# Performance work log

Hardware: AMD Instinct MI355X
Metric: run time of the kernel (lower is better)

The kernel has to match this reference:

```python
import jax, jax.numpy as jnp
import numpy as np

N_EMBD = 1024
N_HEAD = 16


def setup_inputs() -> dict:
    key = jax.random.key(0)
    ks = jax.random.split(key, 9)
    s = 1.0 / np.sqrt(N_EMBD)
    d = {
        "x": jax.random.normal(ks[0], (4, 2048, N_EMBD), dtype=jnp.float32),
        "Wq": jax.random.normal(ks[1], (N_EMBD, N_EMBD), dtype=jnp.float32) * s,
        "bq": jnp.zeros((N_EMBD,), dtype=jnp.float32),
        "Wk": jax.random.normal(ks[2], (N_EMBD, N_EMBD), dtype=jnp.float32) * s,
        "bk": jnp.zeros((N_EMBD,), dtype=jnp.float32),
        "Wv": jax.random.normal(ks[3], (N_EMBD, N_EMBD), dtype=jnp.float32) * s,
        "bv": jnp.zeros((N_EMBD,), dtype=jnp.float32),
        "Wp": jax.random.normal(ks[4], (N_EMBD, N_EMBD), dtype=jnp.float32) * s,
        "bp": jnp.zeros((N_EMBD,), dtype=jnp.float32),
    }
    return d


def reference(x, Wq, bq, Wk, bk, Wv, bv, Wp, bp):
    B, T, C = x.shape
    H = N_HEAD
    D = C // H  # head dim
    # QKV projections -> [B, H, T, D]
    def split_heads(y):
        return y.reshape(B, T, H, D).transpose(0, 2, 1, 3)
    q = split_heads(x @ Wq + bq)
    k = split_heads(x @ Wk + bk)
    v = split_heads(x @ Wv + bv)
    # full (non-causal) attention, scaled by 1/sqrt(D)
    att = jnp.einsum("bhtd,bhsd->bhts", q, k) * (1.0 / np.sqrt(D))
    att = jax.nn.softmax(att, axis=-1)  # dropout is identity (p=0 / eval)
    out = jnp.einsum("bhts,bhsd->bhtd", att, v)
    out = out.transpose(0, 2, 1, 3).reshape(B, T, C)
    return out @ Wp + bp
```

## Files before the change

kernel.cpp:

```cpp
#include <hip/hip_runtime.h>
#include <math.h>

#define B_ 4
#define T_ 2048
#define C_ 1024
#define H_ 16
#define D_ 64
#define M_ (B_ * T_)

#define QSCALE 0.18033688011112042f

using bf16x8 = __attribute__((ext_vector_type(8))) short;
using f32x4  = __attribute__((ext_vector_type(4))) float;

__device__ __forceinline__ unsigned short f2bf(float f) {
  unsigned u = __float_as_uint(f);
  unsigned r = u + 0x7FFFu + ((u >> 16) & 1u);
  return (unsigned short)(r >> 16);
}
__device__ __forceinline__ float bf2f(unsigned short h) {
  return __uint_as_float(((unsigned)h) << 16);
}
__device__ __forceinline__ unsigned cvtpk_bf16(float lo, float hi) {
  unsigned r;
  asm volatile("v_cvt_pk_bf16_f32 %0, %1, %2" : "=v"(r) : "v"(lo), "v"(hi));
  return r;
}

__global__ __launch_bounds__(256) void conv_x(const float* __restrict__ x,
                                              unsigned short* __restrict__ hi,
                                              unsigned short* __restrict__ lo) {
  const size_t i = ((size_t)blockIdx.x * 256 + threadIdx.x) * 4;
  const float4 v = *(const float4*)&x[i];
  ushort4 h, l;
  h.x = f2bf(v.x); l.x = f2bf(v.x - bf2f(h.x));
  h.y = f2bf(v.y); l.y = f2bf(v.y - bf2f(h.y));
  h.z = f2bf(v.z); l.z = f2bf(v.z - bf2f(h.z));
  h.w = f2bf(v.w); l.w = f2bf(v.w - bf2f(h.w));
  *(ushort4*)&hi[i] = h;
  *(ushort4*)&lo[i] = l;
}

__global__ __launch_bounds__(256) void conv_wT(const float* __restrict__ W,
                                               unsigned short* __restrict__ hi,
                                               unsigned short* __restrict__ lo,
                                               int n_off) {
  __shared__ float t[64][65];
  const int k0 = blockIdx.y * 64, n0 = blockIdx.x * 64;
  const int lr = threadIdx.x >> 4;
  const int lc4 = (threadIdx.x & 15) * 4;
#pragma unroll
  for (int i = 0; i < 4; ++i) {
    const int r = lr + 16 * i;
    const float4 v = *(const float4*)&W[(size_t)(k0 + r) * 1024 + n0 + lc4];
    t[r][lc4 + 0] = v.x; t[r][lc4 + 1] = v.y;
    t[r][lc4 + 2] = v.z; t[r][lc4 + 3] = v.w;
  }
  __syncthreads();
#pragma unroll
  for (int i = 0; i < 4; ++i) {
    const int nr = lr + 16 * i;
    ushort4 h, l;
    float a0 = t[lc4 + 0][nr], a1 = t[lc4 + 1][nr];
    float a2 = t[lc4 + 2][nr], a3 = t[lc4 + 3][nr];
    h.x = f2bf(a0); l.x = f2bf(a0 - bf2f(h.x));
    h.y = f2bf(a1); l.y = f2bf(a1 - bf2f(h.y));
    h.z = f2bf(a2); l.z = f2bf(a2 - bf2f(h.z));
    h.w = f2bf(a3); l.w = f2bf(a3 - bf2f(h.w));
    const size_t o = (size_t)(n_off + n0 + nr) * 1024 + k0 + lc4;
    *(ushort4*)&hi[o] = h;
    *(ushort4*)&lo[o] = l;
  }
}

template <int MODE>
__global__ __launch_bounds__(256) void gemm_mfma(
    const unsigned short* __restrict__ Ahi, const unsigned short* __restrict__ Alo,
    const unsigned short* __restrict__ Bhi, const unsigned short* __restrict__ Blo,
    const float* __restrict__ bias0, const float* __restrict__ bias1,
    const float* __restrict__ bias2,
    void* P0, void* P1, void* P2, void* P3, void* P4, void* P5) {
  __shared__ __align__(16) unsigned short AhS[128 * 32];
  __shared__ __align__(16) unsigned short AlS[128 * 32];
  __shared__ __align__(16) unsigned short BhS[128 * 32];
  __shared__ __align__(16) unsigned short BlS[128 * 32];

  const int tid = threadIdx.x;
  const int lane = tid & 63;
  const int wid = tid >> 6;

  const int GX = (MODE == 1) ? 24 : 8;
  const int nwg = GX * 64;
  int lin = blockIdx.x + blockIdx.y * GX;
  lin = (lin & 7) * (nwg >> 3) + (lin >> 3);
  const int m0 = (lin / GX) * 128, n0 = (lin % GX) * 128;

  const int wm = (wid >> 1) * 64, wn = (wid & 1) * 64;

  f32x4 acc[4][4] = {};

  const int srow = lane >> 2;
  const int sc = lane & 3;
  const int fr = lane & 15;
  const int q = lane >> 4;

  for (int k0 = 0; k0 < 1024; k0 += 32) {
    __syncthreads();
#pragma unroll
    for (int c = 0; c < 2; ++c) {
      const int chunk = wid * 2 + c;
      const int row = chunk * 16 + srow;
      const int kch = sc ^ ((row >> 1) & 3);
      const size_t ao = (size_t)(m0 + row) * 1024 + k0 + kch * 8;
      const size_t bo = (size_t)(n0 + row) * 1024 + k0 + kch * 8;
      __builtin_amdgcn_global_load_lds(
          (const __attribute__((address_space(1))) void*)(Ahi + ao),
          (__attribute__((address_space(3))) void*)(AhS + chunk * 512), 16, 0, 0);
      __builtin_amdgcn_global_load_lds(
          (const __attribute__((address_space(1))) void*)(Alo + ao),
          (__attribute__((address_space(3))) void*)(AlS + chunk * 512), 16, 0, 0);
      __builtin_amdgcn_global_load_lds(
          (const __attribute__((address_space(1))) void*)(Bhi + bo),
          (__attribute__((address_space(3))) void*)(BhS + chunk * 512), 16, 0, 0);
      __builtin_amdgcn_global_load_lds(
          (const __attribute__((address_space(1))) void*)(Blo + bo),
          (__attribute__((address_space(3))) void*)(BlS + chunk * 512), 16, 0, 0);
    }
    __syncthreads();

    bf16x8 afh[4], bfh[4], afl[4], bfl[4];
#pragma unroll
    for (int i = 0; i < 4; ++i) {
      const int arow = wm + i * 16 + fr;
      const int aoff = arow * 32 + (q ^ ((arow >> 1) & 3)) * 8;
      afh[i] = *(const bf16x8*)(AhS + aoff);
      const int brow = wn + i * 16 + fr;
      const int boff = brow * 32 + (q ^ ((brow >> 1) & 3)) * 8;
      bfh[i] = *(const bf16x8*)(BhS + boff);
    }
#pragma unroll
    for (int i = 0; i < 4; ++i)
#pragma unroll
      for (int j = 0; j < 4; ++j)
        acc[i][j] = __builtin_amdgcn_mfma_f32_16x16x32_bf16(afh[i], bfh[j], acc[i][j], 0, 0, 0);
#pragma unroll
    for (int i = 0; i < 4; ++i) {
      const int brow = wn + i * 16 + fr;
      bfl[i] = *(const bf16x8*)(BlS + brow * 32 + (q ^ ((brow >> 1) & 3)) * 8);
    }
#pragma unroll
    for (int i = 0; i < 4; ++i)
#pragma unroll
      for (int j = 0; j < 4; ++j)
        acc[i][j] = __builtin_amdgcn_mfma_f32_16x16x32_bf16(afh[i], bfl[j], acc[i][j], 0, 0, 0);
#pragma unroll
    for (int i = 0; i < 4; ++i) {
      const int arow = wm + i * 16 + fr;
      afl[i] = *(const bf16x8*)(AlS + arow * 32 + (q ^ ((arow >> 1) & 3)) * 8);
    }
#pragma unroll
    for (int i = 0; i < 4; ++i)
#pragma unroll
      for (int j = 0; j < 4; ++j)
        acc[i][j] = __builtin_amdgcn_mfma_f32_16x16x32_bf16(afl[i], bfh[j], acc[i][j], 0, 0, 0);
  }

  if (MODE == 0) {
    float* out = (float*)P0;
#pragma unroll
    for (int i = 0; i < 4; ++i)
#pragma unroll
      for (int j = 0; j < 4; ++j)
#pragma unroll
        for (int r = 0; r < 4; ++r) {
          const int m = m0 + wm + i * 16 + q * 4 + r;
          const int n = n0 + wn + j * 16 + fr;
          out[(size_t)m * 1024 + n] = acc[i][j][r] + bias0[n];
        }
  } else {
#pragma unroll
    for (int i = 0; i < 4; ++i) {
#pragma unroll
      for (int j = 0; j < 4; ++j) {
        const int n = n0 + wn + j * 16 + fr;
        const int seg = n >> 10, ww = n & 1023, h = ww >> 6, d = ww & 63;
        const float bv = ((seg == 0) ? bias0 : (seg == 1) ? bias1 : bias2)[ww];
        const int mb = m0 + wm + i * 16 + q * 4;
        const int b = mb >> 11, t0 = mb & 2047;
        unsigned short hv[4], lv[4];
#pragma unroll
        for (int r = 0; r < 4; ++r) {
          float v = acc[i][j][r] + bv;
          if (seg == 0) v *= QSCALE;
          hv[r] = f2bf(v);
          lv[r] = f2bf(v - bf2f(hv[r]));
        }
        if (seg == 2) {
          const size_t o = (((size_t)b * H_ + h) * D_ + d) * T_ + t0;
          ushort4 h4, l4;
          h4.x = hv[0]; h4.y = hv[1]; h4.z = hv[2]; h4.w = hv[3];
          l4.x = lv[0]; l4.y = lv[1]; l4.z = lv[2]; l4.w = lv[3];
          *(ushort4*)&((unsigned short*)P4)[o] = h4;
          *(ushort4*)&((unsigned short*)P5)[o] = l4;
        } else {
          unsigned short* Hq = (unsigned short*)((seg == 0) ? P0 : P2);
          unsigned short* Lq = (unsigned short*)((seg == 0) ? P1 : P3);
          const size_t ob = ((size_t)b * H_ + h) * T_;
#pragma unroll
          for (int r = 0; r < 4; ++r) {
            const size_t o = (ob + t0 + r) * D_ + d;
            Hq[o] = hv[r];
            Lq[o] = lv[r];
          }
        }
      }
    }
  }
}

__global__ __launch_bounds__(256) void flash_mfma(
    const unsigned short* __restrict__ Qhi, const unsigned short* __restrict__ Qlo,
    const unsigned short* __restrict__ Khi, const unsigned short* __restrict__ Klo,
    const unsigned short* __restrict__ Vthi, const unsigned short* __restrict__ Vtlo,
    unsigned short* __restrict__ chi, unsigned short* __restrict__ clo) {
  __shared__ __align__(16) unsigned short KhiS[64 * 64];
  __shared__ __align__(16) unsigned short KloS[64 * 64];
  __shared__ __align__(16) unsigned short VhiS[64 * 64];
  __shared__ __align__(16) unsigned short VloS[64 * 64];
  __shared__ __align__(16) unsigned short PsT[4][32 * 64];

  const int tid = threadIdx.x;
  const int lane = tid & 63;
  const int w = tid >> 6;

  int lin = blockIdx.x + blockIdx.y * 16;
  lin = (lin & 7) * 128 + (lin >> 3);
  const int bh = lin >> 4;
  const int q0 = (lin & 15) * 128;

  const int b = bh >> 4, h = bh & 15;
  const int fr = lane & 15, q = lane >> 4;

  const size_t kbase = (size_t)bh * T_ * D_;
  const size_t vbase = (size_t)bh * D_ * T_;

  bf16x8 qhi[2][2], qlo[2][2];
#pragma unroll
  for (int g = 0; g < 2; ++g)
#pragma unroll
    for (int ks = 0; ks < 2; ++ks) {
      const size_t a = kbase + (size_t)(q0 + w * 32 + g * 16 + fr) * D_ + ks * 32 + q * 8;
      qhi[g][ks] = *(const bf16x8*)(Qhi + a);
      qlo[g][ks] = *(const bf16x8*)(Qlo + a);
    }

  unsigned short* psw = &PsT[w][0];

  f32x4 accO[4][2] = {};
  float lsum[2] = {};

  for (int s0 = 0; s0 < T_; s0 += 64) {
    __syncthreads();
#pragma unroll
    for (int c = 0; c < 2; ++c) {
      const int ci = w * 128 + c * 64 + lane;
      const int row = ci >> 3, slot = ci & 7;
      const int kch = slot ^ (row & 7);
      const int ldsb = (w * 128 + c * 64) * 8;
      const unsigned short* sk = Khi + kbase + (size_t)(s0 + row) * D_ + kch * 8;
      __builtin_amdgcn_global_load_lds(
          (const __attribute__((address_space(1))) void*)sk,
          (__attribute__((address_space(3))) void*)(KhiS + ldsb), 16, 0, 0);
      const unsigned short* sk2 = Klo + kbase + (size_t)(s0 + row) * D_ + kch * 8;
      __builtin_amdgcn_global_load_lds(
          (const __attribute__((address_space(1))) void*)sk2,
          (__attribute__((address_space(3))) void*)(KloS + ldsb), 16, 0, 0);
      const unsigned short* sv = Vthi + vbase + (size_t)row * T_ + s0 + kch * 8;
      __builtin_amdgcn_global_load_lds(
          (const __attribute__((address_space(1))) void*)sv,
          (__attribute__((address_space(3))) void*)(VhiS + ldsb), 16, 0, 0);
      const unsigned short* sv2 = Vtlo + vbase + (size_t)row * T_ + s0 + kch * 8;
      __builtin_amdgcn_global_load_lds(
          (const __attribute__((address_space(1))) void*)sv2,
          (__attribute__((address_space(3))) void*)(VloS + ldsb), 16, 0, 0);
    }
    __syncthreads();

    f32x4 accS[4][2] = {};
#pragma unroll
    for (int sj = 0; sj < 4; ++sj) {
      bf16x8 khf[2], klf[2];
#pragma unroll
      for (int ks = 0; ks < 2; ++ks) {
        const int rs = sj * 16 + fr;
        const int off = rs * 64 + ((ks * 4 + q) ^ (rs & 7)) * 8;
        khf[ks] = *(const bf16x8*)(KhiS + off);
        klf[ks] = *(const bf16x8*)(KloS + off);
      }
#pragma unroll
      for (int g = 0; g < 2; ++g)
#pragma unroll
        for (int ks = 0; ks < 2; ++ks) {
          accS[sj][g] = __builtin_amdgcn_mfma_f32_16x16x32_bf16(khf[ks], qhi[g][ks], accS[sj][g], 0, 0, 0);
          accS[sj][g] = __builtin_amdgcn_mfma_f32_16x16x32_bf16(khf[ks], qlo[g][ks], accS[sj][g], 0, 0, 0);
          accS[sj][g] = __builtin_amdgcn_mfma_f32_16x16x32_bf16(klf[ks], qhi[g][ks], accS[sj][g], 0, 0, 0);
        }
    }

#pragma unroll
    for (int g = 0; g < 2; ++g) {
      const int qc = g * 16 + fr;
#pragma unroll
      for (int sj = 0; sj < 4; ++sj) {
        const float p0 = __builtin_amdgcn_exp2f(accS[sj][g][0]);
        const float p1 = __builtin_amdgcn_exp2f(accS[sj][g][1]);
        const float p2 = __builtin_amdgcn_exp2f(accS[sj][g][2]);
        const float p3 = __builtin_amdgcn_exp2f(accS[sj][g][3]);
        lsum[g] += (p0 + p1) + (p2 + p3);
        uint2 pk;
        pk.x = cvtpk_bf16(p0, p1);
        pk.y = cvtpk_bf16(p2, p3);
        const int off = (qc * 128 + sj * 32 + q * 8) ^ ((fr & 7) << 4);
        *(uint2*)((char*)psw + off) = pk;
      }
    }

    asm volatile("s_waitcnt lgkmcnt(0)" ::: "memory");
    __builtin_amdgcn_sched_barrier(0);

    bf16x8 pb[2][2];
#pragma unroll
    for (int g = 0; g < 2; ++g)
#pragma unroll
      for (int ks = 0; ks < 2; ++ks) {
        const int off = ((g * 16 + fr) * 128 + ks * 64 + q * 16) ^ ((fr & 7) << 4);
        pb[g][ks] = *(const bf16x8*)((char*)psw + off);
      }
#pragma unroll
    for (int j = 0; j < 4; ++j) {
      bf16x8 vh[2], vl[2];
#pragma unroll
      for (int ks = 0; ks < 2; ++ks) {
        const int rd = j * 16 + fr;
        const int off = rd * 64 + ((ks * 4 + q) ^ (rd & 7)) * 8;
        vh[ks] = *(const bf16x8*)(VhiS + off);
        vl[ks] = *(const bf16x8*)(VloS + off);
      }
#pragma unroll
      for (int g = 0; g < 2; ++g)
#pragma unroll
        for (int ks = 0; ks < 2; ++ks) {
          accO[j][g] = __builtin_amdgcn_mfma_f32_16x16x32_bf16(vh[ks], pb[g][ks], accO[j][g], 0, 0, 0);
          accO[j][g] = __builtin_amdgcn_mfma_f32_16x16x32_bf16(vl[ks], pb[g][ks], accO[j][g], 0, 0, 0);
        }
    }
  }

#pragma unroll
  for (int g = 0; g < 2; ++g) {
    float rs = lsum[g];
    rs += __shfl_xor(rs, 16);
    rs += __shfl_xor(rs, 32);
    const float inv = 1.0f / rs;
    const int t = q0 + w * 32 + g * 16 + fr;
    const size_t rowb = ((size_t)b * T_ + t) * C_ + h * D_;
#pragma unroll
    for (int j = 0; j < 4; ++j) {
      ushort4 h4, l4;
      float v0 = accO[j][g][0] * inv, v1 = accO[j][g][1] * inv;
      float v2 = accO[j][g][2] * inv, v3 = accO[j][g][3] * inv;
      h4.x = f2bf(v0); l4.x = f2bf(v0 - bf2f(h4.x));
      h4.y = f2bf(v1); l4.y = f2bf(v1 - bf2f(h4.y));
      h4.z = f2bf(v2); l4.z = f2bf(v2 - bf2f(h4.z));
      h4.w = f2bf(v3); l4.w = f2bf(v3 - bf2f(h4.w));
      const size_t idx = rowb + j * 16 + q * 4;
      *(ushort4*)&chi[idx] = h4;
      *(ushort4*)&clo[idx] = l4;
    }
  }
}

extern "C" void kernel_launch(void* const* d_in, const int* in_sizes, int n_in,
                              void* d_out, int out_size, void* d_ws,
                              size_t ws_size, hipStream_t stream) {
  const float* x = (const float*)d_in[0];
  const float* Wq = (const float*)d_in[1];
  const float* bq = (const float*)d_in[2];
  const float* Wk = (const float*)d_in[3];
  const float* bk = (const float*)d_in[4];
  const float* Wv = (const float*)d_in[5];
  const float* bv = (const float*)d_in[6];
  const float* Wp = (const float*)d_in[7];
  const float* bp = (const float*)d_in[8];
  float* out = (float*)d_out;

  char* w = (char*)d_ws;
  unsigned short* xhi = (unsigned short*)w;     w += (size_t)M_ * C_ * 2;
  unsigned short* xlo = (unsigned short*)w;     w += (size_t)M_ * C_ * 2;
  unsigned short* Wqkv_hi = (unsigned short*)w; w += (size_t)3 * C_ * C_ * 2;
  unsigned short* Wqkv_lo = (unsigned short*)w; w += (size_t)3 * C_ * C_ * 2;
  unsigned short* Wp_hi = (unsigned short*)w;   w += (size_t)C_ * C_ * 2;
  unsigned short* Wp_lo = (unsigned short*)w;   w += (size_t)C_ * C_ * 2;
  unsigned short* Qhi = (unsigned short*)w;     w += (size_t)M_ * C_ * 2;
  unsigned short* Qlo = (unsigned short*)w;     w += (size_t)M_ * C_ * 2;
  unsigned short* Khi = (unsigned short*)w;     w += (size_t)M_ * C_ * 2;
  unsigned short* Klo = (unsigned short*)w;     w += (size_t)M_ * C_ * 2;
  unsigned short* Vthi = (unsigned short*)w;    w += (size_t)M_ * C_ * 2;
  unsigned short* Vtlo = (unsigned short*)w;    w += (size_t)M_ * C_ * 2;
  unsigned short* chi = (unsigned short*)w;     w += (size_t)M_ * C_ * 2;
  unsigned short* clo = (unsigned short*)w;     w += (size_t)M_ * C_ * 2;

  const dim3 blk(256);

  conv_x<<<dim3((M_ * C_) / (4 * 256)), blk, 0, stream>>>(x, xhi, xlo);
  conv_wT<<<dim3(16, 16), blk, 0, stream>>>(Wq, Wqkv_hi, Wqkv_lo, 0);
  conv_wT<<<dim3(16, 16), blk, 0, stream>>>(Wk, Wqkv_hi, Wqkv_lo, 1024);
  conv_wT<<<dim3(16, 16), blk, 0, stream>>>(Wv, Wqkv_hi, Wqkv_lo, 2048);
  conv_wT<<<dim3(16, 16), blk, 0, stream>>>(Wp, Wp_hi, Wp_lo, 0);

  gemm_mfma<1><<<dim3(3072 / 128, M_ / 128), blk, 0, stream>>>(
      xhi, xlo, Wqkv_hi, Wqkv_lo, bq, bk, bv,
      Qhi, Qlo, Khi, Klo, Vthi, Vtlo);

  flash_mfma<<<dim3(T_ / 128, B_ * H_), blk, 0, stream>>>(
      Qhi, Qlo, Khi, Klo, Vthi, Vtlo, chi, clo);

  gemm_mfma<0><<<dim3(1024 / 128, M_ / 128), blk, 0, stream>>>(
      chi, clo, Wp_hi, Wp_lo, bp, bp, bp,
      out, nullptr, nullptr, nullptr, nullptr, nullptr);

  (void)in_sizes; (void)n_in; (void)out_size; (void)ws_size;
}
```

Before: 522.3 us.

## Double-buffer K/V tiles in flash attention with async global-to-LDS prefetch

Doubles the K/V hi/lo LDS buffers and issues the next tile's global_load_lds before computing on the current one. A vmcnt(8) wait plus raw s_barrier replaces the two __syncthreads per iteration, so load latency can overlap the MFMA work. This doubles K/V LDS use (32KB to 64KB plus the P buffers), which may lower occupancy. The manual waitcnt accounting also depends on no other vector-memory ops being in flight.

```diff
diff --git a/kernel.cpp b/kernel.cpp
--- a/kernel.cpp
+++ b/kernel.cpp
@@ -223,10 +223,10 @@
     const unsigned short* __restrict__ Khi, const unsigned short* __restrict__ Klo,
     const unsigned short* __restrict__ Vthi, const unsigned short* __restrict__ Vtlo,
     unsigned short* __restrict__ chi, unsigned short* __restrict__ clo) {
-  __shared__ __align__(16) unsigned short KhiS[64 * 64];
-  __shared__ __align__(16) unsigned short KloS[64 * 64];
-  __shared__ __align__(16) unsigned short VhiS[64 * 64];
-  __shared__ __align__(16) unsigned short VloS[64 * 64];
+  __shared__ __align__(16) unsigned short KhiS[2][64 * 64];
+  __shared__ __align__(16) unsigned short KloS[2][64 * 64];
+  __shared__ __align__(16) unsigned short VhiS[2][64 * 64];
+  __shared__ __align__(16) unsigned short VloS[2][64 * 64];
   __shared__ __align__(16) unsigned short PsT[4][32 * 64];
 
   const int tid = threadIdx.x;
@@ -244,6 +244,51 @@
   const size_t kbase = (size_t)bh * T_ * D_;
   const size_t vbase = (size_t)bh * D_ * T_;
 
+  const int ci0 = w * 128 + lane;
+  const int srow0 = ci0 >> 3, sslot0 = ci0 & 7;
+  const int skch0 = sslot0 ^ (srow0 & 7);
+  const int ci1 = ci0 + 64;
+  const int srow1 = ci1 >> 3, sslot1 = ci1 & 7;
+  const int skch1 = sslot1 ^ (srow1 & 7);
+  const int ldsb0 = (w * 128) * 8;
+  const int ldsb1 = (w * 128 + 64) * 8;
+
+#define STAGE_TILE(buf, s0)                                                      \
+  do {                                                                           \
+    const unsigned short* k0p = Khi + kbase + (size_t)((s0) + srow0) * D_ + skch0 * 8; \
+    const unsigned short* k1p = Klo + kbase + (size_t)((s0) + srow0) * D_ + skch0 * 8; \
+    const unsigned short* v0p = Vthi + vbase + (size_t)srow0 * T_ + (s0) + skch0 * 8;  \
+    const unsigned short* v1p = Vtlo + vbase + (size_t)srow0 * T_ + (s0) + skch0 * 8;  \
+    __builtin_amdgcn_global_load_lds(                                            \
+        (const __attribute__((address_space(1))) void*)k0p,                      \
+        (__attribute__((address_space(3))) void*)(KhiS[buf] + ldsb0), 16, 0, 0); \
+    __builtin_amdgcn_global_load_lds(                                            \
+        (const __attribute__((address_space(1))) void*)k1p,                      \
+        (__attribute__((address_space(3))) void*)(KloS[buf] + ldsb0), 16, 0, 0); \
+    __builtin_amdgcn_global_load_lds(                                            \
+        (const __attribute__((address_space(1))) void*)v0p,                      \
+        (__attribute__((address_space(3))) void*)(VhiS[buf] + ldsb0), 16, 0, 0); \
+    __builtin_amdgcn_global_load_lds(                                            \
+        (const __attribute__((address_space(1))) void*)v1p,                      \
+        (__attribute__((address_space(3))) void*)(VloS[buf] + ldsb0), 16, 0, 0); \
+    const unsigned short* k2p = Khi + kbase + (size_t)((s0) + srow1) * D_ + skch1 * 8; \
+    const unsigned short* k3p = Klo + kbase + (size_t)((s0) + srow1) * D_ + skch1 * 8; \
+    const unsigned short* v2p = Vthi + vbase + (size_t)srow1 * T_ + (s0) + skch1 * 8;  \
+    const unsigned short* v3p = Vtlo + vbase + (size_t)srow1 * T_ + (s0) + skch1 * 8;  \
+    __builtin_amdgcn_global_load_lds(                                            \
+        (const __attribute__((address_space(1))) void*)k2p,                      \
+        (__attribute__((address_space(3))) void*)(KhiS[buf] + ldsb1), 16, 0, 0); \
+    __builtin_amdgcn_global_load_lds(                                            \
+        (const __attribute__((address_space(1))) void*)k3p,                      \
+        (__attribute__((address_space(3))) void*)(KloS[buf] + ldsb1), 16, 0, 0); \
+    __builtin_amdgcn_global_load_lds(                                            \
+        (const __attribute__((address_space(1))) void*)v2p,                      \
+        (__attribute__((address_space(3))) void*)(VhiS[buf] + ldsb1), 16, 0, 0); \
+    __builtin_amdgcn_global_load_lds(                                            \
+        (const __attribute__((address_space(1))) void*)v3p,                      \
+        (__attribute__((address_space(3))) void*)(VloS[buf] + ldsb1), 16, 0, 0); \
+  } while (0)
+
   bf16x8 qhi[2][2], qlo[2][2];
 #pragma unroll
   for (int g = 0; g < 2; ++g)
@@ -259,32 +304,25 @@
   f32x4 accO[4][2] = {};
   float lsum[2] = {};
 
+  STAGE_TILE(0, 0);
+
+  int cur = 0;
   for (int s0 = 0; s0 < T_; s0 += 64) {
-    __syncthreads();
-#pragma unroll
-    for (int c = 0; c < 2; ++c) {
-      const int ci = w * 128 + c * 64 + lane;
-      const int row = ci >> 3, slot = ci & 7;
-      const int kch = slot ^ (row & 7);
-      const int ldsb = (w * 128 + c * 64) * 8;
-      const unsigned short* sk = Khi + kbase + (size_t)(s0 + row) * D_ + kch * 8;
-      __builtin_amdgcn_global_load_lds(
-          (const __attribute__((address_space(1))) void*)sk,
-          (__attribute__((address_space(3))) void*)(KhiS + ldsb), 16, 0, 0);
-      const unsigned short* sk2 = Klo + kbase + (size_t)(s0 + row) * D_ + kch * 8;
-      __builtin_amdgcn_global_load_lds(
-          (const __attribute__((address_space(1))) void*)sk2,
-          (__attribute__((address_space(3))) void*)(KloS + ldsb), 16, 0, 0);
-      const unsigned short* sv = Vthi + vbase + (size_t)row * T_ + s0 + kch * 8;
-      __builtin_amdgcn_global_load_lds(
-          (const __attribute__((address_space(1))) void*)sv,
-          (__attribute__((address_space(3))) void*)(VhiS + ldsb), 16, 0, 0);
-      const unsigned short* sv2 = Vtlo + vbase + (size_t)row * T_ + s0 + kch * 8;
-      __builtin_amdgcn_global_load_lds(
-          (const __attribute__((address_space(1))) void*)sv2,
-          (__attribute__((address_space(3))) void*)(VloS + ldsb), 16, 0, 0);
-    }
-    __syncthreads();
+    const bool more = (s0 + 64) < T_;
+    if (more) {
+      STAGE_TILE(cur ^ 1, s0 + 64);
+      asm volatile("s_waitcnt vmcnt(8)" ::: "memory");
+    } else {
+      asm volatile("s_waitcnt vmcnt(0)" ::: "memory");
+    }
+    __builtin_amdgcn_sched_barrier(0);
+    asm volatile("s_barrier" ::: "memory");
+    __builtin_amdgcn_sched_barrier(0);
+
+    const unsigned short* KhS = KhiS[cur];
+    const unsigned short* KlS = KloS[cur];
+    const unsigned short* VhS = VhiS[cur];
+    const unsigned short* VlS = VloS[cur];
 
     f32x4 accS[4][2] = {};
 #pragma unroll
@@ -294,8 +332,8 @@
       for (int ks = 0; ks < 2; ++ks) {
         const int rs = sj * 16 + fr;
         const int off = rs * 64 + ((ks * 4 + q) ^ (rs & 7)) * 8;
-        khf[ks] = *(const bf16x8*)(KhiS + off);
-        klf[ks] = *(const bf16x8*)(KloS + off);
+        khf[ks] = *(const bf16x8*)(KhS + off);
+        klf[ks] = *(const bf16x8*)(KlS + off);
       }
 #pragma unroll
       for (int g = 0; g < 2; ++g)
@@ -343,8 +381,8 @@
       for (int ks = 0; ks < 2; ++ks) {
         const int rd = j * 16 + fr;
         const int off = rd * 64 + ((ks * 4 + q) ^ (rd & 7)) * 8;
-        vh[ks] = *(const bf16x8*)(VhiS + off);
-        vl[ks] = *(const bf16x8*)(VloS + off);
+        vh[ks] = *(const bf16x8*)(VhS + off);
+        vl[ks] = *(const bf16x8*)(VlS + off);
       }
 #pragma unroll
       for (int g = 0; g < 2; ++g)
@@ -354,6 +392,11 @@
           accO[j][g] = __builtin_amdgcn_mfma_f32_16x16x32_bf16(vl[ks], pb[g][ks], accO[j][g], 0, 0, 0);
         }
     }
+
+    __builtin_amdgcn_sched_barrier(0);
+    asm volatile("s_barrier" ::: "memory");
+    __builtin_amdgcn_sched_barrier(0);
+    cur ^= 1;
   }
 
 #pragma unroll
@@ -378,6 +421,7 @@
       *(ushort4*)&clo[idx] = l4;
     }
   }
+#undef STAGE_TILE
 }
 
 extern "C" void kernel_launch(void* const* d_in, const int* in_sizes, int n_in,
```

Measured after the change: 493.1 us. 5.6% less time.
